# Kernel optimization log

Hardware: AMD Instinct MI355X
Metric: run time of the kernel (lower is better)

## Reference

```python
import jax, jax.numpy as jnp
import numpy as np

NUM_NODES = 2048
EMB = (512, 512, 256)
LATENT = 512
N_FEAT = 512
N_TOTAL = 16384  # batch_size * NUM_NODES
N_EDGES = 524288


def setup_inputs() -> dict:
    key = jax.random.key(0)
    ks = jax.random.split(key, 14)
    s = 0.02
    inp = {
        "x": jax.random.normal(ks[0], (N_TOTAL, N_FEAT), jnp.float32),
        "edge_index": jax.random.randint(ks[1], (2, N_EDGES), 0, N_TOTAL, dtype=jnp.int64),
        "batch_size": 8,
        "batch_index": jax.random.randint(ks[2], (N_TOTAL,), 0, 8, dtype=jnp.int64),
        "W1": jax.random.normal(ks[3], (N_FEAT, EMB[0]), jnp.float32) * s,
        "b1": jnp.zeros((EMB[0],), jnp.float32),
        "W2": jax.random.normal(ks[4], (EMB[0], EMB[1]), jnp.float32) * s,
        "b2": jnp.zeros((EMB[1],), jnp.float32),
        "W3": jax.random.normal(ks[5], (EMB[1], EMB[2]), jnp.float32) * s,
        "b3": jnp.zeros((EMB[2],), jnp.float32),
        "We": jax.random.normal(ks[6], (NUM_NODES * EMB[2], LATENT), jnp.float32) * s,
        "be": jnp.zeros((LATENT,), jnp.float32),
        "Wd": jax.random.normal(ks[7], (LATENT, NUM_NODES), jnp.float32) * s,
        "bd": jnp.zeros((NUM_NODES,), jnp.float32),
    }
    return inp


def reference(x, edge_index, batch_size, batch_index, W1, b1, W2, b2, W3, b3, We, be, Wd, bd):
    N = x.shape[0]
    loops = jnp.arange(N)
    row = jnp.concatenate([edge_index[0], loops])  # sources
    col = jnp.concatenate([edge_index[1], loops])  # targets
    # symmetric degree normalization (PyG GCNConv with self loops)
    deg = jax.ops.segment_sum(jnp.ones_like(col, dtype=x.dtype), col, num_segments=N)
    dinv = jnp.where(deg > 0, jax.lax.rsqrt(deg), jnp.zeros_like(deg))
    norm = (dinv[row] * dinv[col])[:, None]  # [E+N, 1]

    def gcn(h, W, b):
        h = h @ W  # transform first (PyG order)
        return jax.ops.segment_sum(h[row] * norm, col, num_segments=N) + b

    h = jax.nn.relu(gcn(x, W1, b1))
    h = jax.nn.relu(gcn(h, W2, b2))
    h = gcn(h, W3, b3)                      # [N, EMB[2]]
    h = h.reshape(-1, NUM_NODES * EMB[2])   # [batch, NUM_NODES*EMB[2]]
    z = h @ We + be                          # encoder Linear
    out = z @ Wd + bd                        # decoder Linear -> [batch, NUM_NODES]
    return out
```

## Files before the change

kernel.cpp:

```cpp
#include <hip/hip_runtime.h>
#include <stdint.h>

#define NT 16384
#define NN 2048
#define NB 8

typedef __attribute__((ext_vector_type(4))) float f32x4;
typedef __attribute__((ext_vector_type(2))) float f32x2;
typedef __attribute__((ext_vector_type(8))) short s16x8;
typedef __attribute__((ext_vector_type(4))) short s16x4;

__device__ __forceinline__ float bf2f(short u) {
    unsigned v = ((unsigned)(unsigned short)u) << 16;
    return __builtin_bit_cast(float, v);
}
__device__ __forceinline__ short f2bf(float f) {
    unsigned u = __builtin_bit_cast(unsigned, f);
    u += 0x7fffu + ((u >> 16) & 1u);
    return (short)(u >> 16);
}
__device__ __forceinline__ void gload16(const void* g, void* l) {
    __builtin_amdgcn_global_load_lds(
        (const __attribute__((address_space(1))) void*)g,
        (__attribute__((address_space(3))) void*)l, 16, 0, 0);
}
__device__ __forceinline__ long long eidx(const void* ei, long long i, int is64) {
    if (is64) return ((const long long*)ei)[i];
    return (long long)((const int*)ei)[i];
}

__global__ void k_detect(const void* ei, int nchk, int* flag) {
    __shared__ int bad;
    if (threadIdx.x == 0) bad = 0;
    __syncthreads();
    const long long* p = (const long long*)ei;
    for (int i = threadIdx.x; i < nchk; i += 256) {
        long long v = p[i];
        if (v < 0 || v >= NT) bad = 1;
    }
    __syncthreads();
    if (threadIdx.x == 0) *flag = bad ? 0 : 1;
}

__global__ void k_count(const void* ei, int E, const int* flag, int* count) {
    int e = blockIdx.x * 256 + threadIdx.x;
    if (e >= E) return;
    int f = *flag;
    int c = (int)eidx(ei, (long long)E + e, f);
    atomicAdd(&count[c], 1);
}

__global__ __launch_bounds__(1024) void k_scan(const int* __restrict__ count,
        int* __restrict__ offs, float* __restrict__ dinv) {
    __shared__ int ps[1024];
    const int t = threadIdx.x;
    const int base = t * 16;
    int loc[16];
    int s = 0;
#pragma unroll
    for (int j = 0; j < 16; j++) { loc[j] = count[base + j]; s += loc[j]; }
    ps[t] = s;
    __syncthreads();
    for (int o = 1; o < 1024; o <<= 1) {
        int v = (t >= o) ? ps[t - o] : 0;
        __syncthreads();
        ps[t] += v;
        __syncthreads();
    }
    int ex = ps[t] - s;
#pragma unroll
    for (int j = 0; j < 16; j++) {
        offs[base + j] = ex;
        ex += loc[j];
        dinv[base + j] = rsqrtf((float)(loc[j] + 1));
    }
}

__global__ void k_fill(const void* ei, int E, const int* flag,
                       const int* offs, int* cursor, int* csr) {
    int e = blockIdx.x * 256 + threadIdx.x;
    if (e >= E) return;
    int f = *flag;
    int r = (int)eidx(ei, e, f);
    int c = (int)eidx(ei, (long long)E + e, f);
    int pos = offs[c] + atomicAdd(&cursor[c], 1);
    csr[pos] = r;
}

__global__ void k_convw(const float* __restrict__ W, short* __restrict__ Wt,
                        int K, int N) {
    int idx = blockIdx.x * 256 + threadIdx.x;
    if (idx >= K * N) return;
    int k = idx / N, n = idx - k * N;
    Wt[(size_t)n * K + k] = f2bf(W[idx]);
}

__global__ __launch_bounds__(256) void k_scale_x(const float* __restrict__ x,
        const float* __restrict__ dinv, short* __restrict__ xs) {
    int i = blockIdx.x * 256 + threadIdx.x;
    f32x4 v = *(const f32x4*)(x + (size_t)i * 4);
    float d = dinv[i >> 7];
    s16x4 o;
#pragma unroll
    for (int j = 0; j < 4; j++) o[j] = f2bf(v[j] * d);
    *(s16x4*)(xs + (size_t)i * 4) = o;
}

__global__ __launch_bounds__(256) void k_gemm(const short* __restrict__ A,
        const short* __restrict__ Bt, short* __restrict__ Co, int N, int K) {
    __shared__ short As[4096];
    __shared__ short Bs[4096];
    const int t = threadIdx.x;
    const int w = t >> 6, l = t & 63;
    const int row0 = blockIdx.x * 128;
    const int col0 = blockIdx.y * 128;
    const int lr = l & 15, lhi = l >> 4;
    const int wr = (w >> 1) * 64, wc = (w & 1) * 64;
    const int srow = t >> 2;
    const int skoff = (t & 3) * 8;
    const int ldsbase = w * 512;
    f32x4 acc[4][4] = {};
    for (int k0 = 0; k0 < K; k0 += 32) {
#pragma unroll
        for (int i = 0; i < 2; i++) {
            int r = i * 64 + srow;
            gload16(A  + (size_t)(row0 + r) * K + k0 + skoff, (void*)(As + i * 2048 + ldsbase));
            gload16(Bt + (size_t)(col0 + r) * K + k0 + skoff, (void*)(Bs + i * 2048 + ldsbase));
        }
        __syncthreads();
        s16x8 af[4], bfr[4];
#pragma unroll
        for (int m = 0; m < 4; m++) af[m]  = *(const s16x8*)(As + (wr + m * 16 + lr) * 32 + lhi * 8);
#pragma unroll
        for (int n = 0; n < 4; n++) bfr[n] = *(const s16x8*)(Bs + (wc + n * 16 + lr) * 32 + lhi * 8);
#pragma unroll
        for (int m = 0; m < 4; m++)
#pragma unroll
            for (int n = 0; n < 4; n++)
                acc[m][n] = __builtin_amdgcn_mfma_f32_16x16x32_bf16(af[m], bfr[n], acc[m][n], 0, 0, 0);
        __syncthreads();
    }
#pragma unroll
    for (int m = 0; m < 4; m++)
#pragma unroll
        for (int n = 0; n < 4; n++)
#pragma unroll
            for (int j = 0; j < 4; j++) {
                int r = row0 + wr + m * 16 + lhi * 4 + j;
                int c = col0 + wc + n * 16 + lr;
                Co[(size_t)r * N + c] = f2bf(acc[m][n][j]);
            }
}

__global__ __launch_bounds__(256) void k_agg512(const short* __restrict__ T,
        const int* __restrict__ offs, const int* __restrict__ cnt,
        const int* __restrict__ csr, const float* __restrict__ dinv,
        const float* __restrict__ bias, short* __restrict__ H) {
    const int w = threadIdx.x >> 6, l = threadIdx.x & 63;
    const int node = blockIdx.x * 4 + w;
    const int c0 = l * 8;
    const short* base = T + c0;
    float acc[8];
    {
        s16x8 r = *(const s16x8*)(base + (size_t)node * 512);
#pragma unroll
        for (int v = 0; v < 8; v++) acc[v] = bf2f(r[v]);
    }
    const int beg = offs[node], end = beg + cnt[node];
    int j = beg;
    for (; j + 4 <= end; j += 4) {
        int s0 = csr[j], s1 = csr[j + 1], s2 = csr[j + 2], s3 = csr[j + 3];
        s16x8 r0 = *(const s16x8*)(base + (size_t)s0 * 512);
        s16x8 r1 = *(const s16x8*)(base + (size_t)s1 * 512);
        s16x8 r2 = *(const s16x8*)(base + (size_t)s2 * 512);
        s16x8 r3 = *(const s16x8*)(base + (size_t)s3 * 512);
#pragma unroll
        for (int v = 0; v < 8; v++)
            acc[v] += (bf2f(r0[v]) + bf2f(r1[v])) + (bf2f(r2[v]) + bf2f(r3[v]));
    }
    for (; j < end; j++) {
        s16x8 r0 = *(const s16x8*)(base + (size_t)csr[j] * 512);
#pragma unroll
        for (int v = 0; v < 8; v++) acc[v] += bf2f(r0[v]);
    }
    const float dc = dinv[node];
    f32x4 b0 = *(const f32x4*)(bias + c0);
    f32x4 b1 = *(const f32x4*)(bias + c0 + 4);
    s16x8 outv;
#pragma unroll
    for (int v = 0; v < 8; v++) {
        float bb = (v < 4) ? b0[v] : b1[v - 4];
        float o = acc[v] * dc + bb;
        o = fmaxf(o, 0.f);
        o *= dc;
        outv[v] = f2bf(o);
    }
    *(s16x8*)(H + (size_t)node * 512 + c0) = outv;
}

__global__ __launch_bounds__(256) void k_agg256(const short* __restrict__ T,
        const int* __restrict__ offs, const int* __restrict__ cnt,
        const int* __restrict__ csr, const float* __restrict__ dinv,
        const float* __restrict__ bias, float* __restrict__ H3) {
    const int w = threadIdx.x >> 6, l = threadIdx.x & 63;
    const int node = blockIdx.x * 4 + w;
    const int c0 = l * 4;
    const short* base = T + c0;
    float acc[4];
    {
        s16x4 r = *(const s16x4*)(base + (size_t)node * 256);
#pragma unroll
        for (int v = 0; v < 4; v++) acc[v] = bf2f(r[v]);
    }
    const int beg = offs[node], end = beg + cnt[node];
    int j = beg;
    for (; j + 4 <= end; j += 4) {
        int s0 = csr[j], s1 = csr[j + 1], s2 = csr[j + 2], s3 = csr[j + 3];
        s16x4 r0 = *(const s16x4*)(base + (size_t)s0 * 256);
        s16x4 r1 = *(const s16x4*)(base + (size_t)s1 * 256);
        s16x4 r2 = *(const s16x4*)(base + (size_t)s2 * 256);
        s16x4 r3 = *(const s16x4*)(base + (size_t)s3 * 256);
#pragma unroll
        for (int v = 0; v < 4; v++)
            acc[v] += (bf2f(r0[v]) + bf2f(r1[v])) + (bf2f(r2[v]) + bf2f(r3[v]));
    }
    for (; j < end; j++) {
        s16x4 r0 = *(const s16x4*)(base + (size_t)csr[j] * 256);
#pragma unroll
        for (int v = 0; v < 4; v++) acc[v] += bf2f(r0[v]);
    }
    const float dc = dinv[node];
    f32x4 bb = *(const f32x4*)(bias + c0);
    f32x4 o;
#pragma unroll
    for (int v = 0; v < 4; v++) o[v] = acc[v] * dc + bb[v];
    *(f32x4*)(H3 + (size_t)node * 256 + c0) = o;
}

__global__ __launch_bounds__(256) void k_enc(const float* __restrict__ h3,
        const float* __restrict__ We, float* __restrict__ z) {
    __shared__ float hT[512 * 8];
    const int t = threadIdx.x;
    const int k0 = blockIdx.x * 512;
#pragma unroll
    for (int b = 0; b < 8; b++) {
#pragma unroll
        for (int i = 0; i < 2; i++) {
            int k = t + i * 256;
            hT[k * 8 + b] = h3[(size_t)b * 524288 + k0 + k];
        }
    }
    __syncthreads();
    float acc[8][2] = {};
    const float* wp = We + (size_t)k0 * 512 + 2 * t;
    for (int k = 0; k < 512; k++) {
        f32x2 wv = *(const f32x2*)(wp + (size_t)k * 512);
        f32x4 ha = *(const f32x4*)(hT + k * 8);
        f32x4 hb = *(const f32x4*)(hT + k * 8 + 4);
#pragma unroll
        for (int b = 0; b < 4; b++) {
            acc[b][0]     += ha[b] * wv[0];
            acc[b][1]     += ha[b] * wv[1];
            acc[4 + b][0] += hb[b] * wv[0];
            acc[4 + b][1] += hb[b] * wv[1];
        }
    }
#pragma unroll
    for (int b = 0; b < 8; b++) {
        atomicAdd(&z[b * 512 + 2 * t],     acc[b][0]);
        atomicAdd(&z[b * 512 + 2 * t + 1], acc[b][1]);
    }
}

__global__ __launch_bounds__(256) void k_dec(const float* __restrict__ z,
        const float* __restrict__ be, const float* __restrict__ Wd,
        const float* __restrict__ bd, float* __restrict__ out) {
    __shared__ float zs[512];
    const int b = blockIdx.x >> 3;
    const int n = ((blockIdx.x & 7) << 8) + threadIdx.x;
    for (int i = threadIdx.x; i < 512; i += 256) zs[i] = z[b * 512 + i] + be[i];
    __syncthreads();
    float acc = bd[n];
    for (int k = 0; k < 512; k++) acc += zs[k] * Wd[(size_t)k * 2048 + n];
    out[b * 2048 + n] = acc;
}

extern "C" void kernel_launch(void* const* d_in, const int* in_sizes, int n_in,
                              void* d_out, int out_size, void* d_ws, size_t ws_size,
                              hipStream_t stream) {
    const float* x  = (const float*)d_in[0];
    const void*  ei = d_in[1];
    const float* W1 = (const float*)d_in[4];
    const float* b1 = (const float*)d_in[5];
    const float* W2 = (const float*)d_in[6];
    const float* b2 = (const float*)d_in[7];
    const float* W3 = (const float*)d_in[8];
    const float* b3 = (const float*)d_in[9];
    const float* We = (const float*)d_in[10];
    const float* be = (const float*)d_in[11];
    const float* Wd = (const float*)d_in[12];
    const float* bd = (const float*)d_in[13];
    float* out = (float*)d_out;
    const int E = in_sizes[1] / 2;

    char* ws = (char*)d_ws;
    size_t off = 0;
    auto alloc = [&](size_t bytes) {
        void* p = ws + off;
        off = (off + bytes + 255) & ~(size_t)255;
        return p;
    };
    int*   flag   = (int*)  alloc(4);
    int*   count  = (int*)  alloc((size_t)NT * 4);
    int*   offs   = (int*)  alloc((size_t)NT * 4);
    int*   cursor = (int*)  alloc((size_t)NT * 4);
    float* dinv   = (float*)alloc((size_t)NT * 4);
    int*   csr    = (int*)  alloc((size_t)E * 4);
    short* Wt1    = (short*)alloc((size_t)512 * 512 * 2);
    short* Wt2    = (short*)alloc((size_t)512 * 512 * 2);
    short* Wt3    = (short*)alloc((size_t)256 * 512 * 2);
    short* bufA   = (short*)alloc((size_t)NT * 512 * 2);
    short* bufB   = (short*)alloc((size_t)NT * 512 * 2);
    float* z      = (float*)alloc((size_t)NB * 512 * 4);

    hipMemsetAsync(count,  0, (size_t)NT * 4, stream);
    hipMemsetAsync(cursor, 0, (size_t)NT * 4, stream);
    hipMemsetAsync(z,      0, (size_t)NB * 512 * 4, stream);

    k_detect<<<1, 256, 0, stream>>>(ei, 2048, flag);
    k_count<<<(E + 255) / 256, 256, 0, stream>>>(ei, E, flag, count);
    k_scan<<<1, 1024, 0, stream>>>(count, offs, dinv);
    k_fill<<<(E + 255) / 256, 256, 0, stream>>>(ei, E, flag, offs, cursor, csr);

    k_convw<<<(512 * 512) / 256, 256, 0, stream>>>(W1, Wt1, 512, 512);
    k_convw<<<(512 * 512) / 256, 256, 0, stream>>>(W2, Wt2, 512, 512);
    k_convw<<<(512 * 256) / 256, 256, 0, stream>>>(W3, Wt3, 512, 256);
    k_scale_x<<<(NT * 512 / 4) / 256, 256, 0, stream>>>(x, dinv, bufA);

    dim3 g1(128, 4);
    k_gemm<<<g1, 256, 0, stream>>>(bufA, Wt1, bufB, 512, 512);
    k_agg512<<<NT / 4, 256, 0, stream>>>(bufB, offs, count, csr, dinv, b1, bufA);
    k_gemm<<<g1, 256, 0, stream>>>(bufA, Wt2, bufB, 512, 512);
    k_agg512<<<NT / 4, 256, 0, stream>>>(bufB, offs, count, csr, dinv, b2, bufA);
    dim3 g3(128, 2);
    k_gemm<<<g3, 256, 0, stream>>>(bufA, Wt3, bufB, 256, 512);
    k_agg256<<<NT / 4, 256, 0, stream>>>(bufB, offs, count, csr, dinv, b3, (float*)bufA);

    k_enc<<<1024, 256, 0, stream>>>((const float*)bufA, We, z);
    k_dec<<<64, 256, 0, stream>>>(z, be, Wd, bd, out);
}
```

Baseline: 557.9 us.

## Replace encoder atomics with partial-sum reduction, deepen aggregation unroll, merge weight conversion

The encoder GEMV now has each block split K across two thread halves and reduce them in LDS. Each block writes its partial sums to a buffer instead of doing global atomicAdds. A new reduction kernel collapses those partials, and the decoder sums the remaining eight before use. The aggregation loops unroll to eight neighbour gathers per iteration for more memory-level parallelism, the three weight-conversion launches merge into one, and the two memsets merge into one by placing cursor next to count. The partial buffer adds about 16MB of write plus read traffic in exchange for removing atomic contention.

```diff
diff --git a/kernel.cpp b/kernel.cpp
--- a/kernel.cpp
+++ b/kernel.cpp
@@ -87,12 +87,16 @@
     csr[pos] = r;
 }
 
-__global__ void k_convw(const float* __restrict__ W, short* __restrict__ Wt,
-                        int K, int N) {
+__global__ void k_convw_all(const float* __restrict__ W1, const float* __restrict__ W2,
+                            const float* __restrict__ W3, short* __restrict__ Wt1,
+                            short* __restrict__ Wt2, short* __restrict__ Wt3) {
     int idx = blockIdx.x * 256 + threadIdx.x;
-    if (idx >= K * N) return;
-    int k = idx / N, n = idx - k * N;
-    Wt[(size_t)n * K + k] = f2bf(W[idx]);
+    const float* W; short* Wt; int N, base;
+    if (idx < 262144)      { W = W1; Wt = Wt1; N = 512; base = idx; }
+    else if (idx < 524288) { W = W2; Wt = Wt2; N = 512; base = idx - 262144; }
+    else                   { W = W3; Wt = Wt3; N = 256; base = idx - 524288; }
+    int k = base / N, n = base - k * N;
+    Wt[(size_t)n * 512 + k] = f2bf(W[base]);
 }
 
 __global__ __launch_bounds__(256) void k_scale_x(const float* __restrict__ x,
@@ -168,15 +172,28 @@
     }
     const int beg = offs[node], end = beg + cnt[node];
     int j = beg;
-    for (; j + 4 <= end; j += 4) {
-        int s0 = csr[j], s1 = csr[j + 1], s2 = csr[j + 2], s3 = csr[j + 3];
+    for (; j + 8 <= end; j += 8) {
+        int sIx[8];
+#pragma unroll
+        for (int q = 0; q < 8; q++) sIx[q] = csr[j + q];
+        s16x8 r[8];
+#pragma unroll
+        for (int q = 0; q < 8; q++) r[q] = *(const s16x8*)(base + (size_t)sIx[q] * 512);
+#pragma unroll
+        for (int v = 0; v < 8; v++) {
+            float s01 = bf2f(r[0][v]) + bf2f(r[1][v]);
+            float s23 = bf2f(r[2][v]) + bf2f(r[3][v]);
+            float s45 = bf2f(r[4][v]) + bf2f(r[5][v]);
+            float s67 = bf2f(r[6][v]) + bf2f(r[7][v]);
+            acc[v] += (s01 + s23) + (s45 + s67);
+        }
+    }
+    for (; j + 2 <= end; j += 2) {
+        int s0 = csr[j], s1 = csr[j + 1];
         s16x8 r0 = *(const s16x8*)(base + (size_t)s0 * 512);
         s16x8 r1 = *(const s16x8*)(base + (size_t)s1 * 512);
-        s16x8 r2 = *(const s16x8*)(base + (size_t)s2 * 512);
-        s16x8 r3 = *(const s16x8*)(base + (size_t)s3 * 512);
-#pragma unroll
-        for (int v = 0; v < 8; v++)
-            acc[v] += (bf2f(r0[v]) + bf2f(r1[v])) + (bf2f(r2[v]) + bf2f(r3[v]));
+#pragma unroll
+        for (int v = 0; v < 8; v++) acc[v] += bf2f(r0[v]) + bf2f(r1[v]);
     }
     for (; j < end; j++) {
         s16x8 r0 = *(const s16x8*)(base + (size_t)csr[j] * 512);
@@ -214,15 +231,21 @@
     }
     const int beg = offs[node], end = beg + cnt[node];
     int j = beg;
-    for (; j + 4 <= end; j += 4) {
-        int s0 = csr[j], s1 = csr[j + 1], s2 = csr[j + 2], s3 = csr[j + 3];
-        s16x4 r0 = *(const s16x4*)(base + (size_t)s0 * 256);
-        s16x4 r1 = *(const s16x4*)(base + (size_t)s1 * 256);
-        s16x4 r2 = *(const s16x4*)(base + (size_t)s2 * 256);
-        s16x4 r3 = *(const s16x4*)(base + (size_t)s3 * 256);
-#pragma unroll
-        for (int v = 0; v < 4; v++)
-            acc[v] += (bf2f(r0[v]) + bf2f(r1[v])) + (bf2f(r2[v]) + bf2f(r3[v]));
+    for (; j + 8 <= end; j += 8) {
+        int sIx[8];
+#pragma unroll
+        for (int q = 0; q < 8; q++) sIx[q] = csr[j + q];
+        s16x4 r[8];
+#pragma unroll
+        for (int q = 0; q < 8; q++) r[q] = *(const s16x4*)(base + (size_t)sIx[q] * 256);
+#pragma unroll
+        for (int v = 0; v < 4; v++) {
+            float s01 = bf2f(r[0][v]) + bf2f(r[1][v]);
+            float s23 = bf2f(r[2][v]) + bf2f(r[3][v]);
+            float s45 = bf2f(r[4][v]) + bf2f(r[5][v]);
+            float s67 = bf2f(r[6][v]) + bf2f(r[7][v]);
+            acc[v] += (s01 + s23) + (s45 + s67);
+        }
     }
     for (; j < end; j++) {
         s16x4 r0 = *(const s16x4*)(base + (size_t)csr[j] * 256);
@@ -238,47 +261,78 @@
 }
 
 __global__ __launch_bounds__(256) void k_enc(const float* __restrict__ h3,
-        const float* __restrict__ We, float* __restrict__ z) {
+        const float* __restrict__ We, float* __restrict__ part) {
     __shared__ float hT[512 * 8];
+    __shared__ float red[32 * 128];
     const int t = threadIdx.x;
     const int k0 = blockIdx.x * 512;
-#pragma unroll
-    for (int b = 0; b < 8; b++) {
-#pragma unroll
-        for (int i = 0; i < 2; i++) {
-            int k = t + i * 256;
-            hT[k * 8 + b] = h3[(size_t)b * 524288 + k0 + k];
+    for (int i = t; i < 4096; i += 256) {
+        int b = i >> 9, k = i & 511;
+        hT[k * 8 + b] = h3[(size_t)b * 524288 + k0 + k];
+    }
+    __syncthreads();
+    const int col = (t & 127) * 4;
+    const int khalf = t >> 7;
+    float acc[8][4] = {};
+    const float* wp = We + (size_t)(k0 + khalf * 256) * 512 + col;
+    const float* hp = hT + khalf * 256 * 8;
+#pragma unroll 2
+    for (int k = 0; k < 256; k++) {
+        f32x4 wv = *(const f32x4*)(wp + (size_t)k * 512);
+        f32x4 ha = *(const f32x4*)(hp + k * 8);
+        f32x4 hb = *(const f32x4*)(hp + k * 8 + 4);
+#pragma unroll
+        for (int c = 0; c < 4; c++) {
+            acc[0][c] += ha[0] * wv[c];
+            acc[1][c] += ha[1] * wv[c];
+            acc[2][c] += ha[2] * wv[c];
+            acc[3][c] += ha[3] * wv[c];
+            acc[4][c] += hb[0] * wv[c];
+            acc[5][c] += hb[1] * wv[c];
+            acc[6][c] += hb[2] * wv[c];
+            acc[7][c] += hb[3] * wv[c];
         }
     }
-    __syncthreads();
-    float acc[8][2] = {};
-    const float* wp = We + (size_t)k0 * 512 + 2 * t;
-    for (int k = 0; k < 512; k++) {
-        f32x2 wv = *(const f32x2*)(wp + (size_t)k * 512);
-        f32x4 ha = *(const f32x4*)(hT + k * 8);
-        f32x4 hb = *(const f32x4*)(hT + k * 8 + 4);
-#pragma unroll
-        for (int b = 0; b < 4; b++) {
-            acc[b][0]     += ha[b] * wv[0];
-            acc[b][1]     += ha[b] * wv[1];
-            acc[4 + b][0] += hb[b] * wv[0];
-            acc[4 + b][1] += hb[b] * wv[1];
+    if (khalf) {
+#pragma unroll
+        for (int b = 0; b < 8; b++)
+#pragma unroll
+            for (int c = 0; c < 4; c++)
+                red[(b * 4 + c) * 128 + (t - 128)] = acc[b][c];
+    }
+    __syncthreads();
+    if (!khalf) {
+#pragma unroll
+        for (int b = 0; b < 8; b++) {
+            f32x4 o;
+#pragma unroll
+            for (int c = 0; c < 4; c++) o[c] = acc[b][c] + red[(b * 4 + c) * 128 + t];
+            *(f32x4*)(part + (size_t)blockIdx.x * 4096 + b * 512 + col) = o;
         }
     }
-#pragma unroll
-    for (int b = 0; b < 8; b++) {
-        atomicAdd(&z[b * 512 + 2 * t],     acc[b][0]);
-        atomicAdd(&z[b * 512 + 2 * t + 1], acc[b][1]);
-    }
-}
-
-__global__ __launch_bounds__(256) void k_dec(const float* __restrict__ z,
+}
+
+__global__ __launch_bounds__(256) void k_zred(const float* __restrict__ part,
+                                              float* __restrict__ zpart) {
+    const int n = blockIdx.x * 256 + threadIdx.x;
+    const int p0 = blockIdx.y * 128;
+    float s = 0.f;
+    for (int q = 0; q < 128; q++) s += part[(size_t)(p0 + q) * 4096 + n];
+    zpart[(size_t)blockIdx.y * 4096 + n] = s;
+}
+
+__global__ __launch_bounds__(256) void k_dec(const float* __restrict__ zpart,
         const float* __restrict__ be, const float* __restrict__ Wd,
         const float* __restrict__ bd, float* __restrict__ out) {
     __shared__ float zs[512];
     const int b = blockIdx.x >> 3;
     const int n = ((blockIdx.x & 7) << 8) + threadIdx.x;
-    for (int i = threadIdx.x; i < 512; i += 256) zs[i] = z[b * 512 + i] + be[i];
+    for (int i = threadIdx.x; i < 512; i += 256) {
+        float s = be[i];
+#pragma unroll
+        for (int p = 0; p < 8; p++) s += zpart[(size_t)p * 4096 + b * 512 + i];
+        zs[i] = s;
+    }
     __syncthreads();
     float acc = bd[n];
     for (int k = 0; k < 512; k++) acc += zs[k] * Wd[(size_t)k * 2048 + n];
@@ -312,8 +366,8 @@
     };
     int*   flag   = (int*)  alloc(4);
     int*   count  = (int*)  alloc((size_t)NT * 4);
+    int*   cursor = (int*)  alloc((size_t)NT * 4);
     int*   offs   = (int*)  alloc((size_t)NT * 4);
-    int*   cursor = (int*)  alloc((size_t)NT * 4);
     float* dinv   = (float*)alloc((size_t)NT * 4);
     int*   csr    = (int*)  alloc((size_t)E * 4);
     short* Wt1    = (short*)alloc((size_t)512 * 512 * 2);
@@ -321,20 +375,17 @@
     short* Wt3    = (short*)alloc((size_t)256 * 512 * 2);
     short* bufA   = (short*)alloc((size_t)NT * 512 * 2);
     short* bufB   = (short*)alloc((size_t)NT * 512 * 2);
-    float* z      = (float*)alloc((size_t)NB * 512 * 4);
-
-    hipMemsetAsync(count,  0, (size_t)NT * 4, stream);
-    hipMemsetAsync(cursor, 0, (size_t)NT * 4, stream);
-    hipMemsetAsync(z,      0, (size_t)NB * 512 * 4, stream);
+    float* part   = (float*)alloc((size_t)1024 * 4096 * 4);
+    float* zpart  = (float*)alloc((size_t)8 * 4096 * 4);
+
+    hipMemsetAsync(count, 0, (size_t)NT * 8, stream);
 
     k_detect<<<1, 256, 0, stream>>>(ei, 2048, flag);
     k_count<<<(E + 255) / 256, 256, 0, stream>>>(ei, E, flag, count);
     k_scan<<<1, 1024, 0, stream>>>(count, offs, dinv);
     k_fill<<<(E + 255) / 256, 256, 0, stream>>>(ei, E, flag, offs, cursor, csr);
 
-    k_convw<<<(512 * 512) / 256, 256, 0, stream>>>(W1, Wt1, 512, 512);
-    k_convw<<<(512 * 512) / 256, 256, 0, stream>>>(W2, Wt2, 512, 512);
-    k_convw<<<(512 * 256) / 256, 256, 0, stream>>>(W3, Wt3, 512, 256);
+    k_convw_all<<<2560, 256, 0, stream>>>(W1, W2, W3, Wt1, Wt2, Wt3);
     k_scale_x<<<(NT * 512 / 4) / 256, 256, 0, stream>>>(x, dinv, bufA);
 
     dim3 g1(128, 4);
@@ -346,6 +397,8 @@
     k_gemm<<<g3, 256, 0, stream>>>(bufA, Wt3, bufB, 256, 512);
     k_agg256<<<NT / 4, 256, 0, stream>>>(bufB, offs, count, csr, dinv, b3, (float*)bufA);
 
-    k_enc<<<1024, 256, 0, stream>>>((const float*)bufA, We, z);
-    k_dec<<<64, 256, 0, stream>>>(z, be, Wd, bd, out);
-}
+    k_enc<<<1024, 256, 0, stream>>>((const float*)bufA, We, part);
+    dim3 gz(16, 8);
+    k_zred<<<gz, 256, 0, stream>>>(part, zpart);
+    k_dec<<<64, 256, 0, stream>>>(zpart, be, Wd, bd, out);
+}
```

Result: faster. 533.2 us (-4.4%).
